# Kernel optimization log

Measured on AMD Instinct MI355X. Metric: run time of the kernel, lower is better.

The kernel has to match this reference:

```python
import jax, jax.numpy as jnp
import numpy as np

B, S, D = 2, 2048, 1024
H = 16
DH = D // H  # 64

def setup_inputs() -> dict:
    key = jax.random.key(0)
    ks = jax.random.split(key, 7)
    sc = 1.0 / np.sqrt(DH)
    return {
        "sequences": jax.random.normal(ks[0], (B, S, D), dtype=jnp.float32),
        "Wq": jax.random.normal(ks[1], (H, DH, DH), dtype=jnp.float32) * sc,
        "bq": jax.random.normal(ks[2], (H, DH), dtype=jnp.float32) * 0.02,
        "Wk": jax.random.normal(ks[3], (H, DH, DH), dtype=jnp.float32) * sc,
        "bk": jax.random.normal(ks[4], (H, DH), dtype=jnp.float32) * 0.02,
        "Wv": jax.random.normal(ks[5], (H, DH, DH), dtype=jnp.float32) * sc,
        "bv": jax.random.normal(ks[6], (H, DH), dtype=jnp.float32) * 0.02,
    }

def reference(sequences, Wq, bq, Wk, bk, Wv, bv):
    b, s, _ = sequences.shape
    x = sequences.reshape(b, s, H, DH)  # [B,S,H,Dh]
    # torch Linear: y = x @ W^T + b; W is [out,in] => einsum contracts input dim d
    q = jnp.einsum("bshd,hed->bshe", x, Wq) + bq  # [B,S,H,Dh]
    k = jnp.einsum("bshd,hed->bshe", x, Wk) + bk
    v = jnp.einsum("bshd,hed->bshe", x, Wv) + bv
    scores = jnp.einsum("bshd,bthd->bhst", q, k) / jnp.sqrt(jnp.float32(DH))
    attn = jax.nn.softmax(scores, axis=-1)  # [B,H,S,S]
    out = jnp.einsum("bhst,bthd->bshd", attn, v)  # [B,S,H,Dh]
    return out.reshape(b, s, H * DH)
```

## Files before the change

### kernel.cpp

```cpp
#include <hip/hip_runtime.h>

typedef unsigned short u16;
typedef __bf16 bf16x8 __attribute__((ext_vector_type(8)));
typedef float  f32x4  __attribute__((ext_vector_type(4)));
typedef u16    u16x4  __attribute__((ext_vector_type(4)));

#define HH   16
#define DHH  64
#define SEQL 2048
#define NB   2
#define BHN  (NB * HH)
#define SCLF 0.1803368801111204f

static __device__ __forceinline__ u16 f2bf(float f) {
    return __builtin_bit_cast(u16, (__bf16)f);
}

static __device__ __forceinline__ void gload_lds16(const void* g, void* l) {
    __builtin_amdgcn_global_load_lds(
        (const __attribute__((address_space(1))) unsigned int*)g,
        (__attribute__((address_space(3))) unsigned int*)l, 16, 0, 0);
}

__global__ __launch_bounds__(256) void wconv_kernel(
    const float* __restrict__ Wq, const float* __restrict__ Wk,
    const float* __restrict__ Wv, u16* __restrict__ Wb)
{
    const int m = blockIdx.y;
    const float* W = (m == 0) ? Wq : (m == 1) ? Wk : Wv;
    const float s = (m == 0) ? SCLF : 1.0f;
    const int i = (blockIdx.x * 256 + threadIdx.x) * 4;
    float4 v = *reinterpret_cast<const float4*>(W + i);
    u16x4 o = { f2bf(v.x * s), f2bf(v.y * s), f2bf(v.z * s), f2bf(v.w * s) };
    *reinterpret_cast<u16x4*>(Wb + (size_t)m * 65536 + i) = o;
}

__global__ __launch_bounds__(256) void qkv_kernel(
    const float* __restrict__ x, const u16* __restrict__ Wb,
    const float* __restrict__ bq, const float* __restrict__ bk,
    const float* __restrict__ bv,
    u16* __restrict__ Qws, u16* __restrict__ Kws, u16* __restrict__ Vtws)
{
    const int h   = blockIdx.y;
    const int r0  = blockIdx.x * 64;
    const int tid = threadIdx.x;
    const int w   = tid >> 6;
    const int l   = tid & 63;
    const int c   = l & 15;
    const int g   = l >> 4;

    __shared__ u16 vt[64 * 72];

    bf16x8 xa[2];
    {
        const float* xp = x + (size_t)(r0 + w * 16 + c) * 1024 + h * 64 + g * 8;
        #pragma unroll
        for (int kh = 0; kh < 2; ++kh) {
            float4 lo = *reinterpret_cast<const float4*>(xp + kh * 32);
            float4 hi = *reinterpret_cast<const float4*>(xp + kh * 32 + 4);
            bf16x8 f;
            f[0]=(__bf16)lo.x; f[1]=(__bf16)lo.y; f[2]=(__bf16)lo.z; f[3]=(__bf16)lo.w;
            f[4]=(__bf16)hi.x; f[5]=(__bf16)hi.y; f[6]=(__bf16)hi.z; f[7]=(__bf16)hi.w;
            xa[kh] = f;
        }
    }

    const int b      = r0 >> 11;
    const int s_base = r0 & (SEQL - 1);
    const int bh     = b * HH + h;

    const float* bs[3] = {bq + h * 64, bk + h * 64, bv + h * 64};

    #pragma unroll
    for (int m = 0; m < 3; ++m) {
        const u16*   W    = Wb + (size_t)m * 65536 + h * 4096;
        const float* bias = bs[m];
        const float  bscl = (m == 0) ? SCLF : 1.0f;
        f32x4 acc[4];
        #pragma unroll
        for (int ct = 0; ct < 4; ++ct) {
            acc[ct][0] = 0.f; acc[ct][1] = 0.f; acc[ct][2] = 0.f; acc[ct][3] = 0.f;
        }
        #pragma unroll
        for (int kh = 0; kh < 2; ++kh) {
            #pragma unroll
            for (int ct = 0; ct < 4; ++ct) {
                bf16x8 wf = *reinterpret_cast<const bf16x8*>(
                    W + (ct * 16 + c) * 64 + kh * 32 + g * 8);
                acc[ct] = __builtin_amdgcn_mfma_f32_16x16x32_bf16(xa[kh], wf, acc[ct], 0, 0, 0);
            }
        }
        if (m < 2) {
            if (m == 1) __syncthreads();
            #pragma unroll
            for (int ct = 0; ct < 4; ++ct) {
                float bb = bias[ct * 16 + c] * bscl;
                #pragma unroll
                for (int r = 0; r < 4; ++r)
                    vt[(w * 16 + g * 4 + r) * 72 + ct * 16 + c] = f2bf(acc[ct][r] + bb);
            }
            __syncthreads();
            {
                const int d  = tid >> 2;
                const int s0 = (tid & 3) * 16;
                u16* outp = (m == 0 ? Qws : Kws) +
                            ((size_t)bh * SEQL + s_base + d) * 64 + s0;
                uint4 v0 = *reinterpret_cast<const uint4*>(&vt[d * 72 + s0]);
                uint4 v1 = *reinterpret_cast<const uint4*>(&vt[d * 72 + s0 + 8]);
                *reinterpret_cast<uint4*>(outp)     = v0;
                *reinterpret_cast<uint4*>(outp + 8) = v1;
            }
        } else {
            __syncthreads();
            #pragma unroll
            for (int ct = 0; ct < 4; ++ct) {
                float bb = bias[ct * 16 + c];
                u16x4 pb;
                #pragma unroll
                for (int r = 0; r < 4; ++r)
                    pb[r] = f2bf(acc[ct][r] + bb);
                *reinterpret_cast<u16x4*>(&vt[(ct * 16 + c) * 72 + w * 16 + g * 4]) = pb;
            }
            __syncthreads();
            {
                const int d  = tid >> 2;
                const int s0 = (tid & 3) * 16;
                u16* vp = Vtws + ((size_t)bh * 64 + d) * SEQL + s_base + s0;
                uint4 v0 = *reinterpret_cast<const uint4*>(&vt[d * 72 + s0]);
                uint4 v1 = *reinterpret_cast<const uint4*>(&vt[d * 72 + s0 + 8]);
                *reinterpret_cast<uint4*>(vp)     = v0;
                *reinterpret_cast<uint4*>(vp + 8) = v1;
            }
        }
    }
}

__global__ __launch_bounds__(256) void attn_kernel(
    const u16* __restrict__ Qws, const u16* __restrict__ Kws,
    const u16* __restrict__ Vtws, float* __restrict__ out)
{
    const int p     = blockIdx.x;
    const int lid   = (p & 7) * 64 + (p >> 3);
    const int qtile = lid & 15;
    const int bh    = lid >> 4;
    const int b     = bh >> 4;
    const int h     = bh & 15;

    const int tid = threadIdx.x;
    const int w   = tid >> 6;
    const int l   = tid & 63;
    const int c   = l & 15;
    const int g   = l >> 4;
    const int q0  = qtile * 128 + w * 32;

    __shared__ u16 k_lds[2][64 * 64];
    __shared__ u16 v_lds[2][64 * 64];
    __shared__ u16 plds_all[4 * 32 * 64];
    char* pbase = reinterpret_cast<char*>(plds_all + w * (32 * 64));

    const u16* Kb = Kws  + (size_t)bh * SEQL * 64;
    const u16* Vb = Vtws + (size_t)bh * 64 * SEQL;

    const int rs8 = l >> 3;
    const int sx  = (l & 7) ^ rs8;

    #define STAGE(bb, k0)                                                     \
    {   _Pragma("unroll")                                                     \
        for (int a = 0; a < 2; ++a) {                                         \
            const int rbase = w * 16 + a * 8;                                 \
            const int r     = rbase + rs8;                                    \
            gload_lds16(Kb + (size_t)((k0) + r) * 64 + sx * 8,                \
                        &k_lds[bb][rbase * 64]);                              \
            gload_lds16(Vb + (size_t)r * SEQL + (k0) + sx * 8,                \
                        &v_lds[bb][rbase * 64]);                              \
        }                                                                     \
    }

    bf16x8 qf[2][2];
    #pragma unroll
    for (int qt = 0; qt < 2; ++qt)
        #pragma unroll
        for (int kh = 0; kh < 2; ++kh)
            qf[qt][kh] = *reinterpret_cast<const bf16x8*>(
                Qws + ((size_t)bh * SEQL + q0 + qt * 16 + c) * 64 + kh * 32 + g * 8);

    const f32x4 zero4 = {0.f, 0.f, 0.f, 0.f};
    bf16x8 ones8;
    #pragma unroll
    for (int j = 0; j < 8; ++j) ones8[j] = __builtin_bit_cast(__bf16, (u16)0x3F80);

    f32x4 acc[4][2];
    #pragma unroll
    for (int dt = 0; dt < 4; ++dt)
        #pragma unroll
        for (int qt = 0; qt < 2; ++qt) acc[dt][qt] = zero4;
    float mrow[2] = {-1e30f, -1e30f};
    float lrow[2] = {0.f, 0.f};

    const int rdoff = ((g ^ (c & 7)) * 8);

    bf16x8 vfA[8], vfB[8];
    bf16x8 pfA[2][2], pfB[2][2];
    f32x4  suA[2], suB[2];

    STAGE(0, 0);
    __syncthreads();

    auto body = [&](bf16x8 (&vfC)[8], bf16x8 (&pfC)[2][2], f32x4 (&suC)[2],
                    bf16x8 (&vfP)[8], bf16x8 (&pfP)[2][2], f32x4 (&suP)[2],
                    int t, bool has_prev) {
        const int cur = t & 1;

        if (t + 1 < SEQL / 64) STAGE(cur ^ 1, (t + 1) * 64);

        f32x4 st[4][2];
        __builtin_amdgcn_s_setprio(1);
        #pragma unroll
        for (int kt = 0; kt < 4; ++kt) {
            const int e0 = (kt * 16 + c) * 64 + rdoff;
            bf16x8 ka0 = *reinterpret_cast<const bf16x8*>(&k_lds[cur][e0]);
            bf16x8 ka1 = *reinterpret_cast<const bf16x8*>(&k_lds[cur][e0 ^ 32]);
            #pragma unroll
            for (int qt = 0; qt < 2; ++qt) {
                st[kt][qt] = __builtin_amdgcn_mfma_f32_16x16x32_bf16(ka0, qf[qt][0], zero4,      0, 0, 0);
                st[kt][qt] = __builtin_amdgcn_mfma_f32_16x16x32_bf16(ka1, qf[qt][1], st[kt][qt], 0, 0, 0);
            }
        }
        if (has_prev) {
            #pragma unroll
            for (int dt = 0; dt < 4; ++dt)
                #pragma unroll
                for (int qt = 0; qt < 2; ++qt) {
                    acc[dt][qt] = __builtin_amdgcn_mfma_f32_16x16x32_bf16(vfP[dt*2],   pfP[qt][0], acc[dt][qt], 0, 0, 0);
                    acc[dt][qt] = __builtin_amdgcn_mfma_f32_16x16x32_bf16(vfP[dt*2+1], pfP[qt][1], acc[dt][qt], 0, 0, 0);
                }
        }
        __builtin_amdgcn_s_setprio(0);

        #pragma unroll
        for (int dt = 0; dt < 4; ++dt) {
            const int e0 = (dt * 16 + c) * 64 + rdoff;
            vfC[dt * 2]     = *reinterpret_cast<const bf16x8*>(&v_lds[cur][e0]);
            vfC[dt * 2 + 1] = *reinterpret_cast<const bf16x8*>(&v_lds[cur][e0 ^ 32]);
        }

        #pragma unroll
        for (int qt = 0; qt < 2; ++qt) {
            if (has_prev) lrow[qt] += suP[qt][0];

            float a0 = fmaxf(st[0][qt][0], st[0][qt][1]);
            float a1 = fmaxf(st[0][qt][2], st[0][qt][3]);
            float a2 = fmaxf(st[1][qt][0], st[1][qt][1]);
            float a3 = fmaxf(st[1][qt][2], st[1][qt][3]);
            float a4 = fmaxf(st[2][qt][0], st[2][qt][1]);
            float a5 = fmaxf(st[2][qt][2], st[2][qt][3]);
            float a6 = fmaxf(st[3][qt][0], st[3][qt][1]);
            float a7 = fmaxf(st[3][qt][2], st[3][qt][3]);
            float b0 = fmaxf(fmaxf(a0, a1), fmaxf(a2, a3));
            float b1 = fmaxf(fmaxf(a4, a5), fmaxf(a6, a7));
            float mx = fmaxf(b0, b1);
            mx = fmaxf(mx, __shfl_xor(mx, 16, 64));
            mx = fmaxf(mx, __shfl_xor(mx, 32, 64));

            if (!__all(mx <= mrow[qt] + 8.f)) {
                const float mn    = fmaxf(mrow[qt], mx);
                const float alpha = __builtin_amdgcn_exp2f(mrow[qt] - mn);
                mrow[qt] = mn;
                lrow[qt] *= alpha;
                #pragma unroll
                for (int dt = 0; dt < 4; ++dt) {
                    acc[dt][qt][0] *= alpha; acc[dt][qt][1] *= alpha;
                    acc[dt][qt][2] *= alpha; acc[dt][qt][3] *= alpha;
                }
            }

            const int row = qt * 16 + c;
            #pragma unroll
            for (int kt = 0; kt < 4; ++kt) {
                u16x4 pb;
                #pragma unroll
                for (int r = 0; r < 4; ++r)
                    pb[r] = f2bf(__builtin_amdgcn_exp2f(st[kt][qt][r] - mrow[qt]));
                const int blk = (kt * 2 + (g >> 1)) ^ (row & 7);
                *reinterpret_cast<u16x4*>(pbase + row * 128 + blk * 16 + (g & 1) * 8) = pb;
            }
        }

        asm volatile("s_waitcnt lgkmcnt(0)" ::: "memory");

        #pragma unroll
        for (int qt = 0; qt < 2; ++qt) {
            const int row = qt * 16 + c;
            #pragma unroll
            for (int kh = 0; kh < 2; ++kh) {
                const int blk = (kh * 4 + g) ^ (row & 7);
                pfC[qt][kh] = *reinterpret_cast<const bf16x8*>(pbase + row * 128 + blk * 16);
            }
        }
        #pragma unroll
        for (int qt = 0; qt < 2; ++qt) {
            suC[qt] = __builtin_amdgcn_mfma_f32_16x16x32_bf16(ones8, pfC[qt][0], zero4,   0, 0, 0);
            suC[qt] = __builtin_amdgcn_mfma_f32_16x16x32_bf16(ones8, pfC[qt][1], suC[qt], 0, 0, 0);
        }

        __syncthreads();
    };

    for (int tt = 0; tt < SEQL / 64; tt += 2) {
        body(vfA, pfA, suA, vfB, pfB, suB, tt,     tt != 0);
        body(vfB, pfB, suB, vfA, pfA, suA, tt + 1, true);
    }

    #pragma unroll
    for (int dt = 0; dt < 4; ++dt)
        #pragma unroll
        for (int qt = 0; qt < 2; ++qt) {
            acc[dt][qt] = __builtin_amdgcn_mfma_f32_16x16x32_bf16(vfB[dt*2],   pfB[qt][0], acc[dt][qt], 0, 0, 0);
            acc[dt][qt] = __builtin_amdgcn_mfma_f32_16x16x32_bf16(vfB[dt*2+1], pfB[qt][1], acc[dt][qt], 0, 0, 0);
        }
    lrow[0] += suB[0][0];
    lrow[1] += suB[1][0];

    const float inv0 = 1.f / lrow[0];
    const float inv1 = 1.f / lrow[1];
    #pragma unroll
    for (int qt = 0; qt < 2; ++qt) {
        const float inv = qt ? inv1 : inv0;
        float* op = out + ((size_t)b * SEQL + q0 + qt * 16 + c) * 1024 + h * 64 + g * 4;
        #pragma unroll
        for (int dt = 0; dt < 4; ++dt) {
            float4 o;
            o.x = acc[dt][qt][0] * inv; o.y = acc[dt][qt][1] * inv;
            o.z = acc[dt][qt][2] * inv; o.w = acc[dt][qt][3] * inv;
            *reinterpret_cast<float4*>(op + dt * 16) = o;
        }
    }
}

extern "C" void kernel_launch(void* const* d_in, const int* in_sizes, int n_in,
                              void* d_out, int out_size, void* d_ws, size_t ws_size,
                              hipStream_t stream) {
    const float* x  = (const float*)d_in[0];
    const float* Wq = (const float*)d_in[1];
    const float* bq = (const float*)d_in[2];
    const float* Wk = (const float*)d_in[3];
    const float* bk = (const float*)d_in[4];
    const float* Wv = (const float*)d_in[5];
    const float* bv = (const float*)d_in[6];
    float* out = (float*)d_out;

    const size_t per = (size_t)BHN * SEQL * 64;
    u16* Qws = (u16*)d_ws;
    u16* Kws = Qws + per;
    u16* Vt  = Kws + per;
    u16* Wb  = Vt  + per;

    wconv_kernel<<<dim3(64, 3), 256, 0, stream>>>(Wq, Wk, Wv, Wb);
    qkv_kernel<<<dim3(64, 16), 256, 0, stream>>>(x, Wb, bq, bk, bv, Qws, Kws, Vt);
    attn_kernel<<<dim3(512), 256, 0, stream>>>(Qws, Kws, Vt, out);
}
```

Baseline: 85.43 us.

## Switch attention to 32x32x16 MFMA and build P in registers via permlane swap

```diff
diff --git a/kernel.cpp b/kernel.cpp
--- a/kernel.cpp
+++ b/kernel.cpp
@@ -1,9 +1,12 @@
 #include <hip/hip_runtime.h>
 
 typedef unsigned short u16;
+typedef unsigned int   u32;
 typedef __bf16 bf16x8 __attribute__((ext_vector_type(8)));
 typedef float  f32x4  __attribute__((ext_vector_type(4)));
+typedef float  f32x16 __attribute__((ext_vector_type(16)));
 typedef u16    u16x4  __attribute__((ext_vector_type(4)));
+typedef u32    u32x4  __attribute__((ext_vector_type(4)));
 
 #define HH   16
 #define DHH  64
@@ -14,6 +17,12 @@
 
 static __device__ __forceinline__ u16 f2bf(float f) {
     return __builtin_bit_cast(u16, (__bf16)f);
+}
+static __device__ __forceinline__ u32 pack2(float a, float b) {
+    return (u32)f2bf(a) | ((u32)f2bf(b) << 16);
+}
+static __device__ __forceinline__ void plswap(u32 &a, u32 &b) {
+    asm volatile("v_permlane32_swap_b32 %0, %1" : "+v"(a), "+v"(b));
 }
 
 static __device__ __forceinline__ void gload_lds16(const void* g, void* l) {
@@ -135,7 +144,7 @@
     }
 }
 
-__global__ __launch_bounds__(256) void attn_kernel(
+__global__ __launch_bounds__(256, 2) void attn_kernel(
     const u16* __restrict__ Qws, const u16* __restrict__ Kws,
     const u16* __restrict__ Vtws, float* __restrict__ out)
 {
@@ -149,14 +158,12 @@
     const int tid = threadIdx.x;
     const int w   = tid >> 6;
     const int l   = tid & 63;
-    const int c   = l & 15;
-    const int g   = l >> 4;
+    const int lq  = l & 31;
+    const int hi  = l >> 5;
     const int q0  = qtile * 128 + w * 32;
 
     __shared__ u16 k_lds[2][64 * 64];
     __shared__ u16 v_lds[2][64 * 64];
-    __shared__ u16 plds_all[4 * 32 * 64];
-    char* pbase = reinterpret_cast<char*>(plds_all + w * (32 * 64));
 
     const u16* Kb = Kws  + (size_t)bh * SEQL * 64;
     const u16* Vb = Vtws + (size_t)bh * 64 * SEQL;
@@ -176,165 +183,152 @@
         }                                                                     \
     }
 
-    bf16x8 qf[2][2];
-    #pragma unroll
-    for (int qt = 0; qt < 2; ++qt)
-        #pragma unroll
-        for (int kh = 0; kh < 2; ++kh)
-            qf[qt][kh] = *reinterpret_cast<const bf16x8*>(
-                Qws + ((size_t)bh * SEQL + q0 + qt * 16 + c) * 64 + kh * 32 + g * 8);
-
-    const f32x4 zero4 = {0.f, 0.f, 0.f, 0.f};
-    bf16x8 ones8;
-    #pragma unroll
-    for (int j = 0; j < 8; ++j) ones8[j] = __builtin_bit_cast(__bf16, (u16)0x3F80);
-
-    f32x4 acc[4][2];
-    #pragma unroll
-    for (int dt = 0; dt < 4; ++dt)
-        #pragma unroll
-        for (int qt = 0; qt < 2; ++qt) acc[dt][qt] = zero4;
-    float mrow[2] = {-1e30f, -1e30f};
-    float lrow[2] = {0.f, 0.f};
-
-    const int rdoff = ((g ^ (c & 7)) * 8);
-
-    bf16x8 vfA[8], vfB[8];
-    bf16x8 pfA[2][2], pfB[2][2];
-    f32x4  suA[2], suB[2];
+    bf16x8 qf[4];
+    #pragma unroll
+    for (int s = 0; s < 4; ++s)
+        qf[s] = *reinterpret_cast<const bf16x8*>(
+            Qws + ((size_t)bh * SEQL + q0 + lq) * 64 + s * 16 + hi * 8);
+
+    f32x16 zero16;
+    #pragma unroll
+    for (int j = 0; j < 16; ++j) zero16[j] = 0.f;
+
+    f32x16 acc[2];
+    acc[0] = zero16; acc[1] = zero16;
+    float mrow = -1e30f;
+    float lrow = 0.f;
+
+    int koff[4];
+    #pragma unroll
+    for (int s = 0; s < 4; ++s) koff[s] = ((s * 2 + hi) ^ (lq & 7)) * 16;
+
+    bf16x8 vfA[2][4], vfB[2][4];
+    bf16x8 pfA[4], pfB[4];
 
     STAGE(0, 0);
     __syncthreads();
 
-    auto body = [&](bf16x8 (&vfC)[8], bf16x8 (&pfC)[2][2], f32x4 (&suC)[2],
-                    bf16x8 (&vfP)[8], bf16x8 (&pfP)[2][2], f32x4 (&suP)[2],
+    auto body = [&](bf16x8 (&vfC)[2][4], bf16x8 (&pfC)[4],
+                    bf16x8 (&vfP)[2][4], bf16x8 (&pfP)[4],
                     int t, bool has_prev) {
         const int cur = t & 1;
-
         if (t + 1 < SEQL / 64) STAGE(cur ^ 1, (t + 1) * 64);
 
-        f32x4 st[4][2];
+        const char* kb = reinterpret_cast<const char*>(&k_lds[cur][0]);
+        bf16x8 kf0[4], kf1[4];
+        #pragma unroll
+        for (int s = 0; s < 4; ++s) {
+            kf0[s] = *reinterpret_cast<const bf16x8*>(kb + lq * 128 + koff[s]);
+            kf1[s] = *reinterpret_cast<const bf16x8*>(kb + (32 + lq) * 128 + koff[s]);
+        }
+
         __builtin_amdgcn_s_setprio(1);
-        #pragma unroll
-        for (int kt = 0; kt < 4; ++kt) {
-            const int e0 = (kt * 16 + c) * 64 + rdoff;
-            bf16x8 ka0 = *reinterpret_cast<const bf16x8*>(&k_lds[cur][e0]);
-            bf16x8 ka1 = *reinterpret_cast<const bf16x8*>(&k_lds[cur][e0 ^ 32]);
-            #pragma unroll
-            for (int qt = 0; qt < 2; ++qt) {
-                st[kt][qt] = __builtin_amdgcn_mfma_f32_16x16x32_bf16(ka0, qf[qt][0], zero4,      0, 0, 0);
-                st[kt][qt] = __builtin_amdgcn_mfma_f32_16x16x32_bf16(ka1, qf[qt][1], st[kt][qt], 0, 0, 0);
-            }
+        f32x16 st0 = __builtin_amdgcn_mfma_f32_32x32x16_bf16(kf0[0], qf[0], zero16, 0, 0, 0);
+        f32x16 st1 = __builtin_amdgcn_mfma_f32_32x32x16_bf16(kf1[0], qf[0], zero16, 0, 0, 0);
+        #pragma unroll
+        for (int s = 1; s < 4; ++s) {
+            st0 = __builtin_amdgcn_mfma_f32_32x32x16_bf16(kf0[s], qf[s], st0, 0, 0, 0);
+            st1 = __builtin_amdgcn_mfma_f32_32x32x16_bf16(kf1[s], qf[s], st1, 0, 0, 0);
         }
         if (has_prev) {
             #pragma unroll
-            for (int dt = 0; dt < 4; ++dt)
-                #pragma unroll
-                for (int qt = 0; qt < 2; ++qt) {
-                    acc[dt][qt] = __builtin_amdgcn_mfma_f32_16x16x32_bf16(vfP[dt*2],   pfP[qt][0], acc[dt][qt], 0, 0, 0);
-                    acc[dt][qt] = __builtin_amdgcn_mfma_f32_16x16x32_bf16(vfP[dt*2+1], pfP[qt][1], acc[dt][qt], 0, 0, 0);
-                }
+            for (int s = 0; s < 4; ++s) {
+                acc[0] = __builtin_amdgcn_mfma_f32_32x32x16_bf16(vfP[0][s], pfP[s], acc[0], 0, 0, 0);
+                acc[1] = __builtin_amdgcn_mfma_f32_32x32x16_bf16(vfP[1][s], pfP[s], acc[1], 0, 0, 0);
+            }
         }
         __builtin_amdgcn_s_setprio(0);
 
-        #pragma unroll
-        for (int dt = 0; dt < 4; ++dt) {
-            const int e0 = (dt * 16 + c) * 64 + rdoff;
-            vfC[dt * 2]     = *reinterpret_cast<const bf16x8*>(&v_lds[cur][e0]);
-            vfC[dt * 2 + 1] = *reinterpret_cast<const bf16x8*>(&v_lds[cur][e0 ^ 32]);
-        }
-
-        #pragma unroll
-        for (int qt = 0; qt < 2; ++qt) {
-            if (has_prev) lrow[qt] += suP[qt][0];
-
-            float a0 = fmaxf(st[0][qt][0], st[0][qt][1]);
-            float a1 = fmaxf(st[0][qt][2], st[0][qt][3]);
-            float a2 = fmaxf(st[1][qt][0], st[1][qt][1]);
-            float a3 = fmaxf(st[1][qt][2], st[1][qt][3]);
-            float a4 = fmaxf(st[2][qt][0], st[2][qt][1]);
-            float a5 = fmaxf(st[2][qt][2], st[2][qt][3]);
-            float a6 = fmaxf(st[3][qt][0], st[3][qt][1]);
-            float a7 = fmaxf(st[3][qt][2], st[3][qt][3]);
-            float b0 = fmaxf(fmaxf(a0, a1), fmaxf(a2, a3));
-            float b1 = fmaxf(fmaxf(a4, a5), fmaxf(a6, a7));
-            float mx = fmaxf(b0, b1);
-            mx = fmaxf(mx, __shfl_xor(mx, 16, 64));
-            mx = fmaxf(mx, __shfl_xor(mx, 32, 64));
-
-            if (!__all(mx <= mrow[qt] + 8.f)) {
-                const float mn    = fmaxf(mrow[qt], mx);
-                const float alpha = __builtin_amdgcn_exp2f(mrow[qt] - mn);
-                mrow[qt] = mn;
-                lrow[qt] *= alpha;
-                #pragma unroll
-                for (int dt = 0; dt < 4; ++dt) {
-                    acc[dt][qt][0] *= alpha; acc[dt][qt][1] *= alpha;
-                    acc[dt][qt][2] *= alpha; acc[dt][qt][3] *= alpha;
-                }
-            }
-
-            const int row = qt * 16 + c;
-            #pragma unroll
-            for (int kt = 0; kt < 4; ++kt) {
-                u16x4 pb;
-                #pragma unroll
-                for (int r = 0; r < 4; ++r)
-                    pb[r] = f2bf(__builtin_amdgcn_exp2f(st[kt][qt][r] - mrow[qt]));
-                const int blk = (kt * 2 + (g >> 1)) ^ (row & 7);
-                *reinterpret_cast<u16x4*>(pbase + row * 128 + blk * 16 + (g & 1) * 8) = pb;
-            }
-        }
-
-        asm volatile("s_waitcnt lgkmcnt(0)" ::: "memory");
-
-        #pragma unroll
-        for (int qt = 0; qt < 2; ++qt) {
-            const int row = qt * 16 + c;
-            #pragma unroll
-            for (int kh = 0; kh < 2; ++kh) {
-                const int blk = (kh * 4 + g) ^ (row & 7);
-                pfC[qt][kh] = *reinterpret_cast<const bf16x8*>(pbase + row * 128 + blk * 16);
-            }
-        }
-        #pragma unroll
-        for (int qt = 0; qt < 2; ++qt) {
-            suC[qt] = __builtin_amdgcn_mfma_f32_16x16x32_bf16(ones8, pfC[qt][0], zero4,   0, 0, 0);
-            suC[qt] = __builtin_amdgcn_mfma_f32_16x16x32_bf16(ones8, pfC[qt][1], suC[qt], 0, 0, 0);
+        const char* vb = reinterpret_cast<const char*>(&v_lds[cur][0]);
+        #pragma unroll
+        for (int dt = 0; dt < 2; ++dt)
+            #pragma unroll
+            for (int s = 0; s < 4; ++s)
+                vfC[dt][s] = *reinterpret_cast<const bf16x8*>(vb + (dt * 32 + lq) * 128 + koff[s]);
+
+        float t0 = fmaxf(fmaxf(st0[0], st0[1]),  fmaxf(st0[2], st0[3]));
+        float t1 = fmaxf(fmaxf(st0[4], st0[5]),  fmaxf(st0[6], st0[7]));
+        float t2 = fmaxf(fmaxf(st0[8], st0[9]),  fmaxf(st0[10], st0[11]));
+        float t3 = fmaxf(fmaxf(st0[12], st0[13]), fmaxf(st0[14], st0[15]));
+        float t4 = fmaxf(fmaxf(st1[0], st1[1]),  fmaxf(st1[2], st1[3]));
+        float t5 = fmaxf(fmaxf(st1[4], st1[5]),  fmaxf(st1[6], st1[7]));
+        float t6 = fmaxf(fmaxf(st1[8], st1[9]),  fmaxf(st1[10], st1[11]));
+        float t7 = fmaxf(fmaxf(st1[12], st1[13]), fmaxf(st1[14], st1[15]));
+        float mx = fmaxf(fmaxf(fmaxf(t0, t1), fmaxf(t2, t3)),
+                         fmaxf(fmaxf(t4, t5), fmaxf(t6, t7)));
+        mx = fmaxf(mx, __shfl_xor(mx, 32, 64));
+
+        if (!__all(mx <= mrow + 8.f)) {
+            const float mn    = fmaxf(mrow, mx);
+            const float alpha = __builtin_amdgcn_exp2f(mrow - mn);
+            mrow = mn;
+            lrow *= alpha;
+            #pragma unroll
+            for (int j = 0; j < 16; ++j) { acc[0][j] *= alpha; acc[1][j] *= alpha; }
+        }
+
+        float rs0 = 0.f, rs1 = 0.f;
+        u32 wd[16];
+        {
+            float pp[16];
+            #pragma unroll
+            for (int r = 0; r < 16; ++r) {
+                pp[r] = __builtin_amdgcn_exp2f(st0[r] - mrow);
+                if (r & 1) rs1 += pp[r]; else rs0 += pp[r];
+            }
+            #pragma unroll
+            for (int j = 0; j < 8; ++j) wd[j] = pack2(pp[2 * j], pp[2 * j + 1]);
+        }
+        {
+            float pp[16];
+            #pragma unroll
+            for (int r = 0; r < 16; ++r) {
+                pp[r] = __builtin_amdgcn_exp2f(st1[r] - mrow);
+                if (r & 1) rs1 += pp[r]; else rs0 += pp[r];
+            }
+            #pragma unroll
+            for (int j = 0; j < 8; ++j) wd[8 + j] = pack2(pp[2 * j], pp[2 * j + 1]);
+        }
+        lrow += rs0 + rs1;
+
+        plswap(wd[0],  wd[2]);  plswap(wd[1],  wd[3]);
+        plswap(wd[4],  wd[6]);  plswap(wd[5],  wd[7]);
+        plswap(wd[8],  wd[10]); plswap(wd[9],  wd[11]);
+        plswap(wd[12], wd[14]); plswap(wd[13], wd[15]);
+
+        #pragma unroll
+        for (int s = 0; s < 4; ++s) {
+            u32x4 tmp = { wd[s * 4 + 0], wd[s * 4 + 1], wd[s * 4 + 2], wd[s * 4 + 3] };
+            pfC[s] = __builtin_bit_cast(bf16x8, tmp);
         }
 
         __syncthreads();
     };
 
     for (int tt = 0; tt < SEQL / 64; tt += 2) {
-        body(vfA, pfA, suA, vfB, pfB, suB, tt,     tt != 0);
-        body(vfB, pfB, suB, vfA, pfA, suA, tt + 1, true);
-    }
-
-    #pragma unroll
-    for (int dt = 0; dt < 4; ++dt)
-        #pragma unroll
-        for (int qt = 0; qt < 2; ++qt) {
-            acc[dt][qt] = __builtin_amdgcn_mfma_f32_16x16x32_bf16(vfB[dt*2],   pfB[qt][0], acc[dt][qt], 0, 0, 0);
-            acc[dt][qt] = __builtin_amdgcn_mfma_f32_16x16x32_bf16(vfB[dt*2+1], pfB[qt][1], acc[dt][qt], 0, 0, 0);
-        }
-    lrow[0] += suB[0][0];
-    lrow[1] += suB[1][0];
-
-    const float inv0 = 1.f / lrow[0];
-    const float inv1 = 1.f / lrow[1];
-    #pragma unroll
-    for (int qt = 0; qt < 2; ++qt) {
-        const float inv = qt ? inv1 : inv0;
-        float* op = out + ((size_t)b * SEQL + q0 + qt * 16 + c) * 1024 + h * 64 + g * 4;
-        #pragma unroll
-        for (int dt = 0; dt < 4; ++dt) {
+        body(vfA, pfA, vfB, pfB, tt,     tt != 0);
+        body(vfB, pfB, vfA, pfA, tt + 1, true);
+    }
+
+    #pragma unroll
+    for (int s = 0; s < 4; ++s) {
+        acc[0] = __builtin_amdgcn_mfma_f32_32x32x16_bf16(vfB[0][s], pfB[s], acc[0], 0, 0, 0);
+        acc[1] = __builtin_amdgcn_mfma_f32_32x32x16_bf16(vfB[1][s], pfB[s], acc[1], 0, 0, 0);
+    }
+    const float inv = 1.f / (lrow + __shfl_xor(lrow, 32, 64));
+
+    float* op = out + ((size_t)b * SEQL + q0 + lq) * 1024 + h * 64 + hi * 4;
+    #pragma unroll
+    for (int dt = 0; dt < 2; ++dt)
+        #pragma unroll
+        for (int rg = 0; rg < 4; ++rg) {
             float4 o;
-            o.x = acc[dt][qt][0] * inv; o.y = acc[dt][qt][1] * inv;
-            o.z = acc[dt][qt][2] * inv; o.w = acc[dt][qt][3] * inv;
-            *reinterpret_cast<float4*>(op + dt * 16) = o;
-        }
-    }
+            o.x = acc[dt][rg * 4 + 0] * inv;
+            o.y = acc[dt][rg * 4 + 1] * inv;
+            o.z = acc[dt][rg * 4 + 2] * inv;
+            o.w = acc[dt][rg * 4 + 3] * inv;
+            *reinterpret_cast<float4*>(op + dt * 32 + rg * 8) = o;
+        }
 }
 
 extern "C" void kernel_launch(void* const* d_in, const int* in_sizes, int n_in,
```

New measurement: 84.90 us. About the same (-0.6%).
